# Optimization experiments

Hardware: AMD Instinct MI355X
Metric: run time of the kernel (lower is better)

The kernel has to match this reference:

```python
import jax, jax.numpy as jnp
import numpy as np

B, S, H, E, TOP_K = 4, 2048, 1024, 16, 4


def setup_inputs() -> dict:
    key = jax.random.key(0)
    ks = jax.random.split(key, 12)
    sc = 1.0 / np.sqrt(H)
    inp = {
        "x": jax.random.normal(ks[0], (B, S, H), dtype=jnp.float32),
        "image": jax.random.normal(ks[1], (B, S, H), dtype=jnp.float32),
        "text": jax.random.normal(ks[2], (B, S, H), dtype=jnp.float32),
        "audio": jax.random.normal(ks[3], (B, S, H), dtype=jnp.float32),
        # generalized router linear
        "Wg": jax.random.uniform(ks[4], (H, E), jnp.float32, -sc, sc),
        "bg": jax.random.uniform(ks[5], (E,), jnp.float32, -sc, sc),
        # per-modality router linears
        "Wi": jax.random.uniform(ks[6], (H, E), jnp.float32, -sc, sc),
        "bi": jax.random.uniform(ks[7], (E,), jnp.float32, -sc, sc),
        "Wt": jax.random.uniform(ks[8], (H, E), jnp.float32, -sc, sc),
        "bt": jax.random.uniform(ks[9], (E,), jnp.float32, -sc, sc),
        "Wa": jax.random.uniform(ks[10], (H, E), jnp.float32, -sc, sc),
        "ba": jax.random.uniform(ks[11], (E,), jnp.float32, -sc, sc),
    }
    return inp


def reference(x, image, text, audio, Wg, bg, Wi, bi, Wt, bt, Wa, ba):
    # combined_logits = generalized_router(x) + sum_m modality_router_m(modality_m)
    logits = (
        jnp.einsum("bsh,he->bse", x, Wg) + bg
        + jnp.einsum("bsh,he->bse", image, Wi) + bi
        + jnp.einsum("bsh,he->bse", text, Wt) + bt
        + jnp.einsum("bsh,he->bse", audio, Wa) + ba
    )  # [B,S,E]
    router_probs = jax.nn.softmax(logits, axis=-1)
    top_k_probs, top_k_indices = jax.lax.top_k(router_probs, TOP_K)
    top_k_probs = top_k_probs / jnp.sum(top_k_probs, axis=-1, keepdims=True)
    prob_per_expert = jnp.mean(router_probs, axis=(0, 1))  # [E]
    aux_loss = jnp.sum(prob_per_expert * jnp.log(prob_per_expert * E + 1e-9))
    return (top_k_indices, top_k_probs, aux_loss)
```

## Files before the change

kernel.cpp:

```cpp
#include <hip/hip_runtime.h>
#include <math.h>

constexpr int kTokens = 8192;
constexpr int kH      = 1024;
constexpr int kE      = 16;
constexpr int kTopK   = 4;
constexpr int kNC     = 16;

__global__ __launch_bounds__(256, 5)
void router_fmac(const float* __restrict__ x,   const float* __restrict__ img,
                 const float* __restrict__ txt, const float* __restrict__ aud,
                 const float* __restrict__ Wg,  const float* __restrict__ Wi,
                 const float* __restrict__ Wt,  const float* __restrict__ Wa,
                 float* __restrict__ partials)
{
    __shared__ float smem[2 * 4 * 64 * 12];

    const int t  = threadIdx.x;
    const int w  = __builtin_amdgcn_readfirstlane(t >> 6);
    const int ln = t & 63;
    const int hs    = blockIdx.x & 15;
    const int tg    = blockIdx.x >> 4;
    const int tok0  = tg * 64;
    const int hbase = hs * 64;

    const float* Xs[4] = { x,  img, txt, aud };
    const float* Ws[4] = { Wg, Wi,  Wt,  Wa  };

    const int c2 = ln & 1;
    const int rA = ln >> 1;

    float* wbuf0 = smem + w * 768;
    float* wbuf1 = smem + 3072 + w * 768;

    {
        const float* src = Xs[0] + (size_t)(tok0 + rA) * kH + hbase + w * 8 + c2 * 4;
        const float4 va = *(const float4*)(src);
        const float4 vb = *(const float4*)(src + (size_t)32 * kH);
        *(float4*)&wbuf0[rA * 12 + c2 * 4]        = va;
        *(float4*)&wbuf0[(rA + 32) * 12 + c2 * 4] = vb;
    }
    asm volatile("s_waitcnt lgkmcnt(0)" ::: "memory");
    __builtin_amdgcn_sched_barrier(0);

    double dacc[kE];
#pragma unroll
    for (int e = 0; e < kE; ++e) dacc[e] = 0.0;
    float facc[kE];

#pragma unroll
    for (int p = 0; p < 8; ++p) {
        const int m = p >> 1;
        const int s = p & 1;

        float4 na, nb;
        if (p < 7) {
            const int m2 = (p + 1) >> 1, s2 = (p + 1) & 1;
            const float* src = Xs[m2] + (size_t)(tok0 + rA) * kH + hbase + s2 * 32 + w * 8 + c2 * 4;
            na = *(const float4*)(src);
            nb = *(const float4*)(src + (size_t)32 * kH);
        }

        if (s == 0) {
#pragma unroll
            for (int e = 0; e < kE; ++e) facc[e] = 0.f;
        }

        const float* buf   = (p & 1) ? wbuf1 : wbuf0;
        const float* wbase = Ws[m] + (size_t)(hbase + s * 32 + w * 8) * kE;

#pragma unroll
        for (int k4 = 0; k4 < 2; ++k4) {
            const float4 xv = *(const float4*)&buf[ln * 12 + k4 * 4];
#pragma unroll
            for (int j = 0; j < 4; ++j) {
                const float xh = (j == 0) ? xv.x : (j == 1) ? xv.y : (j == 2) ? xv.z : xv.w;
                const float* wr = wbase + (k4 * 4 + j) * kE;
                const float4 w0 = *(const float4*)(wr + 0);
                const float4 w1 = *(const float4*)(wr + 4);
                const float4 w2 = *(const float4*)(wr + 8);
                const float4 w3 = *(const float4*)(wr + 12);
                facc[0]  += xh * w0.x;  facc[1]  += xh * w0.y;
                facc[2]  += xh * w0.z;  facc[3]  += xh * w0.w;
                facc[4]  += xh * w1.x;  facc[5]  += xh * w1.y;
                facc[6]  += xh * w1.z;  facc[7]  += xh * w1.w;
                facc[8]  += xh * w2.x;  facc[9]  += xh * w2.y;
                facc[10] += xh * w2.z;  facc[11] += xh * w2.w;
                facc[12] += xh * w3.x;  facc[13] += xh * w3.y;
                facc[14] += xh * w3.z;  facc[15] += xh * w3.w;
            }
        }

        if (s == 1) {
#pragma unroll
            for (int e = 0; e < kE; ++e) dacc[e] += (double)facc[e];
        }

        if (p < 7) {
            float* nbuf = (p & 1) ? wbuf0 : wbuf1;
            *(float4*)&nbuf[rA * 12 + c2 * 4]        = na;
            *(float4*)&nbuf[(rA + 32) * 12 + c2 * 4] = nb;
        }
        asm volatile("s_waitcnt lgkmcnt(0)" ::: "memory");
        __builtin_amdgcn_sched_barrier(0);
    }

    __syncthreads();
#pragma unroll
    for (int q = 0; q < 4; ++q) {
        *(float4*)&smem[(w * 64 + ln) * 20 + q * 4] =
            make_float4((float)dacc[q * 4 + 0], (float)dacc[q * 4 + 1],
                        (float)dacc[q * 4 + 2], (float)dacc[q * 4 + 3]);
    }
    __syncthreads();
    {
        const int tok = t >> 2;
        const int eq  = t & 3;
        double s0 = 0.0, s1 = 0.0, s2 = 0.0, s3 = 0.0;
#pragma unroll
        for (int ww = 0; ww < 4; ++ww) {
            const float4 v = *(const float4*)&smem[(ww * 64 + tok) * 20 + eq * 4];
            s0 += (double)v.x;  s1 += (double)v.y;
            s2 += (double)v.z;  s3 += (double)v.w;
        }
        *(float4*)&partials[((size_t)hs * kTokens + tok0 + tok) * kE + eq * 4] =
            make_float4((float)s0, (float)s1, (float)s2, (float)s3);
    }
}

__global__ __launch_bounds__(256)
void router_topk(const float* __restrict__ partials,
                 const float* __restrict__ bg, const float* __restrict__ bi,
                 const float* __restrict__ bt, const float* __restrict__ ba,
                 float* __restrict__ out, float* __restrict__ blocksum)
{
    __shared__ double lgs[32][2][kE + 2];
    __shared__ float  pr[32][kE + 1];

    const int t    = threadIdx.x;
    const int tq   = t >> 3;
    const int eq   = (t >> 1) & 3;
    const int hc   = t & 1;
    const int tok0 = blockIdx.x * 32;

    double a0 = 0.0, a1 = 0.0, a2 = 0.0, a3 = 0.0;
    if (hc == 0) {
        a0 = (double)bg[eq*4+0] + (double)bi[eq*4+0] + (double)bt[eq*4+0] + (double)ba[eq*4+0];
        a1 = (double)bg[eq*4+1] + (double)bi[eq*4+1] + (double)bt[eq*4+1] + (double)ba[eq*4+1];
        a2 = (double)bg[eq*4+2] + (double)bi[eq*4+2] + (double)bt[eq*4+2] + (double)ba[eq*4+2];
        a3 = (double)bg[eq*4+3] + (double)bi[eq*4+3] + (double)bt[eq*4+3] + (double)ba[eq*4+3];
    }

#pragma unroll
    for (int c8 = 0; c8 < 8; ++c8) {
        const int c = hc * 8 + c8;
        const float4 v = *(const float4*)(partials + ((size_t)c * kTokens + tok0 + tq) * kE + eq * 4);
        a0 += (double)v.x;  a1 += (double)v.y;  a2 += (double)v.z;  a3 += (double)v.w;
    }
    lgs[tq][hc][eq*4+0] = a0;  lgs[tq][hc][eq*4+1] = a1;
    lgs[tq][hc][eq*4+2] = a2;  lgs[tq][hc][eq*4+3] = a3;
    __syncthreads();

    if (t < 32) {
        const int tok = tok0 + t;
        double lg[kE];
#pragma unroll
        for (int e = 0; e < kE; ++e) lg[e] = lgs[t][0][e] + lgs[t][1][e];

        double mx = lg[0];
#pragma unroll
        for (int e = 1; e < kE; ++e) mx = fmax(mx, lg[e]);

        float p[kE];
        float sum = 0.f;
#pragma unroll
        for (int e = 0; e < kE; ++e) {
            p[e] = expf((float)(lg[e] - mx));
            sum += p[e];
        }
        const float inv = 1.f / sum;
#pragma unroll
        for (int e = 0; e < kE; ++e) { p[e] *= inv; pr[t][e] = p[e]; }

        unsigned used = 0;
        float tp[kTopK];
        int   ti[kTopK];
        float s4 = 0.f;
#pragma unroll
        for (int k = 0; k < kTopK; ++k) {
            float best = -1.f;
            int   bidx = 0;
#pragma unroll
            for (int e = 0; e < kE; ++e) {
                if (!((used >> e) & 1u) && p[e] > best) { best = p[e]; bidx = e; }
            }
            used |= 1u << bidx;
            tp[k] = best;
            ti[k] = bidx;
            s4 += best;
        }
        const float rn = 1.f / s4;

        *(float4*)&out[(size_t)tok * kTopK] =
            make_float4((float)ti[0], (float)ti[1], (float)ti[2], (float)ti[3]);
        *(float4*)&out[(size_t)kTokens * kTopK + (size_t)tok * kTopK] =
            make_float4(tp[0] * rn, tp[1] * rn, tp[2] * rn, tp[3] * rn);
    }
    __syncthreads();

    if (t < kE) {
        float s = 0.f;
#pragma unroll
        for (int tk = 0; tk < 32; ++tk) s += pr[tk][t];
        blocksum[blockIdx.x * kE + t] = s;
    }
}

__global__ __launch_bounds__(256)
void router_aux(const float* __restrict__ blocksum, float* __restrict__ out)
{
    __shared__ double ps[16][kE];
    __shared__ double fin[kE];
    const int t = threadIdx.x;
    {
        const int e  = t & 15;
        const int bq = t >> 4;
        double s = 0.0;
#pragma unroll
        for (int k = 0; k < 16; ++k)
            s += (double)blocksum[(bq * 16 + k) * kE + e];
        ps[bq][e] = s;
    }
    __syncthreads();
    if (t < kE) {
        double s = 0.0;
#pragma unroll
        for (int q = 0; q < 16; ++q) s += ps[q][t];
        fin[t] = s / (double)kTokens;
    }
    __syncthreads();
    if (t == 0) {
        double aux = 0.0;
#pragma unroll
        for (int e = 0; e < kE; ++e) aux += fin[e] * log(fin[e] * (double)kE + 1e-9);
        out[(size_t)kTokens * kTopK * 2] = (float)aux;
    }
}

extern "C" void kernel_launch(void* const* d_in, const int* in_sizes, int n_in,
                              void* d_out, int out_size, void* d_ws, size_t ws_size,
                              hipStream_t stream)
{
    const float* x   = (const float*)d_in[0];
    const float* img = (const float*)d_in[1];
    const float* txt = (const float*)d_in[2];
    const float* aud = (const float*)d_in[3];
    const float* Wg  = (const float*)d_in[4];
    const float* bg  = (const float*)d_in[5];
    const float* Wi  = (const float*)d_in[6];
    const float* bi  = (const float*)d_in[7];
    const float* Wt  = (const float*)d_in[8];
    const float* bt  = (const float*)d_in[9];
    const float* Wa  = (const float*)d_in[10];
    const float* ba  = (const float*)d_in[11];

    float* out      = (float*)d_out;
    float* partials = (float*)d_ws;
    float* blocksum = (float*)((char*)d_ws + (size_t)kNC * kTokens * kE * 4);

    router_fmac<<<2048, 256, 0, stream>>>(x, img, txt, aud, Wg, Wi, Wt, Wa, partials);
    router_topk<<<256, 256, 0, stream>>>(partials, bg, bi, bt, ba, out, blocksum);
    router_aux<<<1, 256, 0, stream>>>(blocksum, out);
}
```

Measured before the change: 187.4 us.

## Deepen global-load prefetch to three stages and make partials token-major

Replaces the single-stage prefetch loop with a hand-unrolled schedule that keeps three pairs of global loads in flight, so each HBM read has more time to land before its data is written to LDS. The LDS row stride drops from 12 to 8 floats, which shrinks the shared-memory footprint but may raise bank conflicts. The partials buffer is reordered to token-major so the top-k kernel reads one contiguous region per token. The extra in-flight registers could push register pressure against the launch-bounds occupancy target.

```diff
diff --git a/kernel.cpp b/kernel.cpp
--- a/kernel.cpp
+++ b/kernel.cpp
@@ -14,7 +14,7 @@
                  const float* __restrict__ Wt,  const float* __restrict__ Wa,
                  float* __restrict__ partials)
 {
-    __shared__ float smem[2 * 4 * 64 * 12];
+    __shared__ float smem[5120];
 
     const int t  = threadIdx.x;
     const int w  = __builtin_amdgcn_readfirstlane(t >> 6);
@@ -30,80 +30,73 @@
     const int c2 = ln & 1;
     const int rA = ln >> 1;
 
-    float* wbuf0 = smem + w * 768;
-    float* wbuf1 = smem + 3072 + w * 768;
-
-    {
-        const float* src = Xs[0] + (size_t)(tok0 + rA) * kH + hbase + w * 8 + c2 * 4;
-        const float4 va = *(const float4*)(src);
-        const float4 vb = *(const float4*)(src + (size_t)32 * kH);
-        *(float4*)&wbuf0[rA * 12 + c2 * 4]        = va;
-        *(float4*)&wbuf0[(rA + 32) * 12 + c2 * 4] = vb;
-    }
-    asm volatile("s_waitcnt lgkmcnt(0)" ::: "memory");
-    __builtin_amdgcn_sched_barrier(0);
+    const size_t loff = (size_t)(tok0 + rA) * kH + hbase + w * 8 + c2 * 4;
+
+    float* wb0 = smem + w * 512;
+    float* wb1 = smem + 2048 + w * 512;
+
+    float4 A0, A1, B0, B1, C0, C1;
+
+#define ISSUE(Rx, Ry, p) { \
+    const float* s_ = Xs[(p) >> 1] + loff + ((p) & 1) * 32; \
+    Rx = *(const float4*)(s_); \
+    Ry = *(const float4*)(s_ + (size_t)32 * kH); }
+
+#define TWRITE(bufp, Rx, Ry) { \
+    *(float4*)&(bufp)[rA * 8 + c2 * 4]        = Rx; \
+    *(float4*)&(bufp)[(rA + 32) * 8 + c2 * 4] = Ry; }
+
+#define FENCE() { asm volatile("s_waitcnt lgkmcnt(0)" ::: "memory"); \
+                  __builtin_amdgcn_sched_barrier(0); }
 
     double dacc[kE];
 #pragma unroll
     for (int e = 0; e < kE; ++e) dacc[e] = 0.0;
     float facc[kE];
 
-#pragma unroll
-    for (int p = 0; p < 8; ++p) {
-        const int m = p >> 1;
-        const int s = p & 1;
-
-        float4 na, nb;
-        if (p < 7) {
-            const int m2 = (p + 1) >> 1, s2 = (p + 1) & 1;
-            const float* src = Xs[m2] + (size_t)(tok0 + rA) * kH + hbase + s2 * 32 + w * 8 + c2 * 4;
-            na = *(const float4*)(src);
-            nb = *(const float4*)(src + (size_t)32 * kH);
-        }
-
-        if (s == 0) {
-#pragma unroll
-            for (int e = 0; e < kE; ++e) facc[e] = 0.f;
-        }
-
-        const float* buf   = (p & 1) ? wbuf1 : wbuf0;
-        const float* wbase = Ws[m] + (size_t)(hbase + s * 32 + w * 8) * kE;
-
-#pragma unroll
-        for (int k4 = 0; k4 < 2; ++k4) {
-            const float4 xv = *(const float4*)&buf[ln * 12 + k4 * 4];
-#pragma unroll
-            for (int j = 0; j < 4; ++j) {
-                const float xh = (j == 0) ? xv.x : (j == 1) ? xv.y : (j == 2) ? xv.z : xv.w;
-                const float* wr = wbase + (k4 * 4 + j) * kE;
-                const float4 w0 = *(const float4*)(wr + 0);
-                const float4 w1 = *(const float4*)(wr + 4);
-                const float4 w2 = *(const float4*)(wr + 8);
-                const float4 w3 = *(const float4*)(wr + 12);
-                facc[0]  += xh * w0.x;  facc[1]  += xh * w0.y;
-                facc[2]  += xh * w0.z;  facc[3]  += xh * w0.w;
-                facc[4]  += xh * w1.x;  facc[5]  += xh * w1.y;
-                facc[6]  += xh * w1.z;  facc[7]  += xh * w1.w;
-                facc[8]  += xh * w2.x;  facc[9]  += xh * w2.y;
-                facc[10] += xh * w2.z;  facc[11] += xh * w2.w;
-                facc[12] += xh * w3.x;  facc[13] += xh * w3.y;
-                facc[14] += xh * w3.z;  facc[15] += xh * w3.w;
-            }
-        }
-
-        if (s == 1) {
-#pragma unroll
-            for (int e = 0; e < kE; ++e) dacc[e] += (double)facc[e];
-        }
-
-        if (p < 7) {
-            float* nbuf = (p & 1) ? wbuf0 : wbuf1;
-            *(float4*)&nbuf[rA * 12 + c2 * 4]        = na;
-            *(float4*)&nbuf[(rA + 32) * 12 + c2 * 4] = nb;
-        }
-        asm volatile("s_waitcnt lgkmcnt(0)" ::: "memory");
-        __builtin_amdgcn_sched_barrier(0);
-    }
+#define RESET() { _Pragma("unroll") for (int e = 0; e < kE; ++e) facc[e] = 0.f; }
+#define FOLD()  { _Pragma("unroll") for (int e = 0; e < kE; ++e) dacc[e] += (double)facc[e]; }
+
+#define COMPUTE(bufp, p) { \
+    const float* wbase = Ws[(p) >> 1] + (size_t)(hbase + ((p) & 1) * 32 + w * 8) * kE; \
+    _Pragma("unroll") for (int k4 = 0; k4 < 2; ++k4) { \
+        const float4 xv = *(const float4*)&(bufp)[ln * 8 + k4 * 4]; \
+        _Pragma("unroll") for (int j = 0; j < 4; ++j) { \
+            const float xh = (j == 0) ? xv.x : (j == 1) ? xv.y : (j == 2) ? xv.z : xv.w; \
+            const float* wr = wbase + (k4 * 4 + j) * kE;    \
+            const float4 w0 = *(const float4*)(wr + 0); \
+            const float4 w1 = *(const float4*)(wr + 4); \
+            const float4 w2 = *(const float4*)(wr + 8); \
+            const float4 w3 = *(const float4*)(wr + 12); \
+            facc[0]  += xh * w0.x;  facc[1]  += xh * w0.y; \
+            facc[2]  += xh * w0.z;  facc[3]  += xh * w0.w; \
+            facc[4]  += xh * w1.x;  facc[5]  += xh * w1.y; \
+            facc[6]  += xh * w1.z;  facc[7]  += xh * w1.w; \
+            facc[8]  += xh * w2.x;  facc[9]  += xh * w2.y; \
+            facc[10] += xh * w2.z;  facc[11] += xh * w2.w; \
+            facc[12] += xh * w3.x;  facc[13] += xh * w3.y; \
+            facc[14] += xh * w3.z;  facc[15] += xh * w3.w; \
+        } } }
+
+    ISSUE(A0, A1, 0);  ISSUE(B0, B1, 1);  ISSUE(C0, C1, 2);
+    TWRITE(wb0, A0, A1);
+    FENCE();
+
+    TWRITE(wb1, B0, B1);  ISSUE(A0, A1, 3);  RESET(); COMPUTE(wb0, 0);          FENCE();
+    TWRITE(wb0, C0, C1);  ISSUE(B0, B1, 4);           COMPUTE(wb1, 1);  FOLD(); FENCE();
+    TWRITE(wb1, A0, A1);  ISSUE(C0, C1, 5);  RESET(); COMPUTE(wb0, 2);          FENCE();
+    TWRITE(wb0, B0, B1);  ISSUE(A0, A1, 6);           COMPUTE(wb1, 3);  FOLD(); FENCE();
+    TWRITE(wb1, C0, C1);  ISSUE(B0, B1, 7);  RESET(); COMPUTE(wb0, 4);          FENCE();
+    TWRITE(wb0, A0, A1);                              COMPUTE(wb1, 5);  FOLD(); FENCE();
+    TWRITE(wb1, B0, B1);                     RESET(); COMPUTE(wb0, 6);          FENCE();
+                                                      COMPUTE(wb1, 7);  FOLD();
+
+#undef ISSUE
+#undef TWRITE
+#undef FENCE
+#undef RESET
+#undef FOLD
+#undef COMPUTE
 
     __syncthreads();
 #pragma unroll
@@ -123,7 +116,7 @@
             s0 += (double)v.x;  s1 += (double)v.y;
             s2 += (double)v.z;  s3 += (double)v.w;
         }
-        *(float4*)&partials[((size_t)hs * kTokens + tok0 + tok) * kE + eq * 4] =
+        *(float4*)&partials[((size_t)(tok0 + tok) * kNC + hs) * kE + eq * 4] =
             make_float4((float)s0, (float)s1, (float)s2, (float)s3);
     }
 }
@@ -154,7 +147,8 @@
 #pragma unroll
     for (int c8 = 0; c8 < 8; ++c8) {
         const int c = hc * 8 + c8;
-        const float4 v = *(const float4*)(partials + ((size_t)c * kTokens + tok0 + tq) * kE + eq * 4);
+        const float4 v = *(const float4*)(partials +
+            ((size_t)(tok0 + tq) * kNC + c) * kE + eq * 4);
         a0 += (double)v.x;  a1 += (double)v.y;  a2 += (double)v.z;  a3 += (double)v.w;
     }
     lgs[tq][hc][eq*4+0] = a0;  lgs[tq][hc][eq*4+1] = a1;
@@ -266,7 +260,7 @@
 
     float* out      = (float*)d_out;
     float* partials = (float*)d_ws;
-    float* blocksum = (float*)((char*)d_ws + (size_t)kNC * kTokens * kE * 4);
+    float* blocksum = (float*)((char*)d_ws + (size_t)kTokens * kNC * kE * 4);
 
     router_fmac<<<2048, 256, 0, stream>>>(x, img, txt, aud, Wg, Wi, Wt, Wa, partials);
     router_topk<<<256, 256, 0, stream>>>(partials, bg, bi, bt, ba, out, blocksum);
```

After: 197.5 us. 1.05x slower.
